# Optimization experiments

Measured on AMD Instinct MI355X. Metric: run time of the kernel, lower is better.

The kernel has to match this reference:

```python
import jax, jax.numpy as jnp
import numpy as np
from jax import lax

B, N, NPOINT, NSAMPLE = 4, 8192, 2048, 32
IN_CH = 64
MLP = (64, 64, 128)
RADIUS = 0.2
BN_EPS = 1e-5
BIG = 1e10


def _fps(xyz, npoint):
    # Farthest point sampling; deterministic start at index 0 (torch uses random start).
    b, n, _ = xyz.shape

    def body(carry, _):
        dist, far = carry
        cen = jnp.take_along_axis(xyz, far[:, None, None], axis=1)  # (B,1,3)
        d = jnp.sum((xyz - cen) ** 2, axis=-1)                      # (B,N)
        dist = jnp.minimum(dist, d)
        return (dist, jnp.argmax(dist, axis=-1).astype(jnp.int32)), far

    init = (jnp.full((b, n), BIG, xyz.dtype), jnp.zeros((b,), jnp.int32))
    _, cents = lax.scan(body, init, None, length=npoint)            # (npoint,B)
    return jnp.transpose(cents)                                     # (B,npoint)


def _sqdist(src, dst):
    # |src|^2 + |dst|^2 - 2 src.dst, clamped at 0 (matches square_distance)
    d = (jnp.sum(src ** 2, -1, keepdims=True)
         + jnp.sum(dst ** 2, -1, keepdims=True).swapaxes(1, 2)
         - 2.0 * jnp.einsum('bsc,bnc->bsn', src, dst))
    return jnp.maximum(d, 0.0)


def _ball_query(radius, nsample, xyz, new_xyz):
    sq = _sqdist(new_xyz, xyz)                           # (B,S,N)
    masked = jnp.where(sq > radius ** 2, BIG, sq)
    _, gidx = lax.top_k(-masked, nsample)                # nsample smallest dists
    gath = jnp.take_along_axis(sq, gidx, axis=2)
    # replace out-of-radius neighbors with the closest (first) neighbor
    return jnp.where(gath > radius ** 2, gidx[:, :, :1], gidx)


def _gather(points, idx):
    # points (B,N,C), idx (B,...) -> (B,...,C)
    return jax.vmap(lambda p, i: p[i])(points, idx)


def _forward(xyz, features, layers):
    fps_idx = _fps(xyz, NPOINT)                          # (B,S)
    new_xyz = _gather(xyz, fps_idx)                      # (B,S,3)
    idx = _ball_query(RADIUS, NSAMPLE, xyz, new_xyz)     # (B,S,K)
    g_xyz = _gather(xyz, idx) - new_xyz[:, :, None, :]   # (B,S,K,3) centered
    g_feat = _gather(features, idx)                      # (B,S,K,C)
    h = jnp.concatenate([g_xyz, g_feat], axis=-1)        # (B,S,K,3+C)
    for (W, g, b, m, v) in layers:                       # conv1x1 + BN(eval) + ReLU
        h = jnp.einsum('bskc,oc->bsko', h, W)
        h = jax.nn.relu((h - m) / jnp.sqrt(v + BN_EPS) * g + b)
    return new_xyz, jnp.max(h, axis=2)                   # max over neighbors K


def setup_inputs() -> dict:
    key = jax.random.key(0)
    ks = jax.random.split(key, 20)
    inp = {
        'xyz': jax.random.uniform(ks[0], (B, N, 3), jnp.float32),
        'features': jax.random.normal(ks[1], (B, N, IN_CH), jnp.float32),
    }
    last = IN_CH + 3
    k = 2
    for i, out in enumerate(MLP):
        inp[f'W{i}'] = jax.random.normal(ks[k], (out, last), jnp.float32) / np.sqrt(last); k += 1
        inp[f'gamma{i}'] = jax.random.uniform(ks[k], (out,), jnp.float32, 0.5, 1.5); k += 1
        inp[f'beta{i}'] = 0.1 * jax.random.normal(ks[k], (out,), jnp.float32); k += 1
        inp[f'mean{i}'] = 0.1 * jax.random.normal(ks[k], (out,), jnp.float32); k += 1
        inp[f'var{i}'] = jax.random.uniform(ks[k], (out,), jnp.float32, 0.5, 1.5); k += 1
        last = out
    return inp


def reference(xyz, features, W0, gamma0, beta0, mean0, var0, W1, gamma1, beta1, mean1, var1, W2, gamma2, beta2, mean2, var2):
    layers = [(W0, gamma0, beta0, mean0, var0),
              (W1, gamma1, beta1, mean1, var1),
              (W2, gamma2, beta2, mean2, var2)]
    return _forward(xyz, features, layers)
```

## Files before the change

kernel.cpp:

```cpp
#include <hip/hip_runtime.h>
#include <cstdint>

#define NPTS 8192
#define NBATCH 4
#define NS 2048
#define NK 32
#define CIN 64
#define C0 67
#define H1 64
#define H2 64
#define H3 128
#define CAP 1024
#define BIGF 1e10f

#define WT0_OFF 0
#define B0_OFF  4288
#define WT1_OFF 4352
#define B1_OFF  8448
#define WT2_OFF 8512
#define B2_OFF  16704
#define FPS_OFF 16832

typedef float f32x2 __attribute__((ext_vector_type(2)));

__device__ __forceinline__ float sq3(float ax, float ay, float az) {
  return __fadd_rn(__fadd_rn(__fmul_rn(ax, ax), __fmul_rn(ay, ay)), __fmul_rn(az, az));
}

__device__ __forceinline__ f32x2 pk_sub(f32x2 a, f32x2 b) {
  f32x2 r;
  asm("v_pk_add_f32 %0, %1, %2 neg_lo:[0,1] neg_hi:[0,1]" : "=v"(r) : "v"(a), "v"(b));
  return r;
}
__device__ __forceinline__ f32x2 pk_mul(f32x2 a, f32x2 b) {
  f32x2 r;
  asm("v_pk_mul_f32 %0, %1, %2" : "=v"(r) : "v"(a), "v"(b));
  return r;
}
__device__ __forceinline__ f32x2 pk_add(f32x2 a, f32x2 b) {
  f32x2 r;
  asm("v_pk_add_f32 %0, %1, %2" : "=v"(r) : "v"(a), "v"(b));
  return r;
}

#define PAIRRED(dv, iv, ctrl)                                                          \
  {                                                                                    \
    int _sd = __builtin_amdgcn_update_dpp(__float_as_int(dv), __float_as_int(dv),      \
                                          (ctrl), 0xf, 0xf, false);                    \
    int _si = __builtin_amdgcn_update_dpp((iv), (iv), (ctrl), 0xf, 0xf, false);        \
    float _fd = __int_as_float(_sd);                                                   \
    bool _tk = (_fd > (dv)) || ((_fd == (dv)) && (_si < (iv)));                        \
    (dv) = _tk ? _fd : (dv);                                                           \
    (iv) = _tk ? _si : (iv);                                                           \
  }

__global__ void fold_kernel(const float* __restrict__ W0, const float* __restrict__ g0, const float* __restrict__ be0, const float* __restrict__ m0, const float* __restrict__ v0,
                            const float* __restrict__ W1, const float* __restrict__ g1, const float* __restrict__ be1, const float* __restrict__ m1, const float* __restrict__ v1,
                            const float* __restrict__ W2, const float* __restrict__ g2, const float* __restrict__ be2, const float* __restrict__ m2, const float* __restrict__ v2,
                            float* __restrict__ ws) {
  int t = blockIdx.x * 256 + threadIdx.x;
  if (t < C0 * H1) {
    int c = t / H1, o = t - c * H1;
    float sc = g0[o] / sqrtf(v0[o] + 1e-5f);
    ws[WT0_OFF + t] = W0[o * C0 + c] * sc;
  } else if (t < B0_OFF + H1) {
    int o = t - B0_OFF;
    float sc = g0[o] / sqrtf(v0[o] + 1e-5f);
    ws[t] = be0[o] - m0[o] * sc;
  } else if (t < WT1_OFF + H1 * H2) {
    int t2 = t - WT1_OFF; int c = t2 / H2, o = t2 - c * H2;
    float sc = g1[o] / sqrtf(v1[o] + 1e-5f);
    ws[t] = W1[o * H1 + c] * sc;
  } else if (t < B1_OFF + H2) {
    int o = t - B1_OFF;
    float sc = g1[o] / sqrtf(v1[o] + 1e-5f);
    ws[t] = be1[o] - m1[o] * sc;
  } else if (t < WT2_OFF + H2 * H3) {
    int t2 = t - WT2_OFF; int c = t2 / H3, o = t2 - c * H3;
    float sc = g2[o] / sqrtf(v2[o] + 1e-5f);
    ws[t] = W2[o * H2 + c] * sc;
  } else if (t < B2_OFF + H3) {
    int o = t - B2_OFF;
    float sc = g2[o] / sqrtf(v2[o] + 1e-5f);
    ws[t] = be2[o] - m2[o] * sc;
  }
}

__global__ __launch_bounds__(256, 1)
void fps_kernel(const float* __restrict__ xyz, float* __restrict__ newxyz, int* __restrict__ fpsidx) {
  const int b = blockIdx.x;
  const float* px = xyz + (size_t)b * NPTS * 3;
  const int tid = threadIdx.x;
  const int lane = tid & 63;
  const int wv = tid >> 6;

  __shared__ __align__(16) float lco[NPTS * 4];
  __shared__ __align__(8) float cnd[2][4][2];

  f32x2 X2[16], Y2[16], Z2[16], D2[16];
#pragma unroll
  for (int jj = 0; jj < 16; ++jj) {
    int p0 = tid * 32 + 2 * jj;
    float x0 = px[p0 * 3 + 0], y0 = px[p0 * 3 + 1], z0 = px[p0 * 3 + 2];
    float x1 = px[p0 * 3 + 3], y1 = px[p0 * 3 + 4], z1 = px[p0 * 3 + 5];
    X2[jj][0] = x0; X2[jj][1] = x1;
    Y2[jj][0] = y0; Y2[jj][1] = y1;
    Z2[jj][0] = z0; Z2[jj][1] = z1;
    D2[jj][0] = BIGF; D2[jj][1] = BIGF;
    *(float4*)&lco[(size_t)p0 * 4]       = make_float4(x0, y0, z0, 0.0f);
    *(float4*)&lco[(size_t)(p0 + 1) * 4] = make_float4(x1, y1, z1, 0.0f);
  }

  float cx = px[0], cy = px[1], cz = px[2];
  if (tid == 0) {
    fpsidx[b * NS] = 0;
    float* o = newxyz + (size_t)b * NS * 3;
    o[0] = cx; o[1] = cy; o[2] = cz;
  }
  __syncthreads();

  int par = 0;
  for (int t = 1; t < NS; ++t) {
    f32x2 cpx, cpy, cpz;
    cpx[0] = cx; cpx[1] = cx;
    cpy[0] = cy; cpy[1] = cy;
    cpz[0] = cz; cpz[1] = cz;
    float bd = -1.0f; int bi = 0;
#pragma unroll
    for (int jj = 0; jj < 16; ++jj) {
      f32x2 dx = pk_sub(X2[jj], cpx);
      f32x2 dy = pk_sub(Y2[jj], cpy);
      f32x2 dz = pk_sub(Z2[jj], cpz);
      f32x2 xx = pk_mul(dx, dx);
      f32x2 yy = pk_mul(dy, dy);
      f32x2 ss = pk_add(xx, yy);
      f32x2 zz = pk_mul(dz, dz);
      f32x2 dd = pk_add(ss, zz);
      float n0 = fminf(D2[jj][0], dd[0]);
      float n1 = fminf(D2[jj][1], dd[1]);
      D2[jj][0] = n0; D2[jj][1] = n1;
      bool g0 = n0 > bd;
      bd = g0 ? n0 : bd;
      bi = g0 ? (tid * 32 + 2 * jj) : bi;
      bool g1 = n1 > bd;
      bd = g1 ? n1 : bd;
      bi = g1 ? (tid * 32 + 2 * jj + 1) : bi;
    }
    PAIRRED(bd, bi, 0x121);
    PAIRRED(bd, bi, 0x122);
    PAIRRED(bd, bi, 0x124);
    PAIRRED(bd, bi, 0x128);
    PAIRRED(bd, bi, 0x142);
    PAIRRED(bd, bi, 0x143);
    if (lane == 63) {
      cnd[par][wv][0] = bd;
      cnd[par][wv][1] = __int_as_float(bi);
    }
    __syncthreads();

    const int ci = lane & 3;
    f32x2 cc = *(const f32x2*)&cnd[par][ci][0];
    float pd = cc[0];
    int pi = __float_as_int(cc[1]);
    PAIRRED(pd, pi, 0x121);
    PAIRRED(pd, pi, 0x122);
    const int far = __builtin_amdgcn_readfirstlane(pi);
    float4 c4 = *(const float4*)&lco[(size_t)far * 4];
    cx = c4.x; cy = c4.y; cz = c4.z;
    if (tid == 0) {
      fpsidx[b * NS + t] = far;
      float* o = newxyz + ((size_t)b * NS + t) * 3;
      o[0] = cx; o[1] = cy; o[2] = cz;
    }
    par ^= 1;
  }
}

__global__ __launch_bounds__(256)
void sa_kernel(const float* __restrict__ xyz, const float* __restrict__ feat,
               const float* __restrict__ ws, const int* __restrict__ fpsidx,
               const float* __restrict__ newxyz, float* __restrict__ outf) {
  const int bs = blockIdx.x;
  const int b = bs >> 11;
  const int s = bs & (NS - 1);
  const int tid = threadIdx.x;
  const int lane = tid & 63;

  __shared__ __align__(16) unsigned long long cand[CAP];
  __shared__ int cntS;
  __shared__ int sel[NK];
  __shared__ float hA[32 * 69];
  __shared__ float hB[32 * 65];

  const float* px = xyz + (size_t)b * NPTS * 3;
  const float* pf = feat + (size_t)b * NPTS * CIN;
  const size_t srow = (size_t)b * NS + s;
  const float cx = newxyz[srow * 3 + 0];
  const float cy = newxyz[srow * 3 + 1];
  const float cz = newxyz[srow * 3 + 2];

  if (tid == 0) cntS = 0;
  __syncthreads();

  const float ssrc = sq3(cx, cy, cz);
  const float R2F = 0.04f;
  for (int p = tid; p < NPTS; p += 256) {
    float x = px[p * 3 + 0], y = px[p * 3 + 1], z = px[p * 3 + 2];
    float sdst = sq3(x, y, z);
    float dot = __fadd_rn(__fadd_rn(__fmul_rn(cx, x), __fmul_rn(cy, y)), __fmul_rn(cz, z));
    float d = __fsub_rn(__fadd_rn(ssrc, sdst), __fmul_rn(2.0f, dot));
    d = fmaxf(d, 0.0f);
    bool hit = (d <= R2F);
    unsigned long long m = __ballot(hit);
    if (m) {
      int base = 0;
      if (lane == 0) base = atomicAdd(&cntS, __popcll(m));
      base = __shfl(base, 0);
      if (hit) {
        int pos = base + __popcll(m & ((1ull << lane) - 1ull));
        if (pos < CAP)
          cand[pos] = ((unsigned long long)__float_as_uint(d) << 32) | (unsigned long long)(unsigned)p;
      }
    }
  }
  __syncthreads();

  {
    const int cnt = min(cntS, CAP);
    if (cnt <= 256) {
      unsigned long long k0 = (tid < cnt) ? cand[tid] : ~0ull;
      int r0 = 0;
      int j = 0;
      for (; j + 2 <= cnt; j += 2) {
        ulonglong2 kj = *(const ulonglong2*)&cand[j];
        r0 += (kj.x < k0) ? 1 : 0;
        r0 += (kj.y < k0) ? 1 : 0;
      }
      if (j < cnt) r0 += (cand[j] < k0) ? 1 : 0;
      if (tid < cnt) {
        if (r0 < NK) sel[r0] = (int)(k0 & 0xffffffffull);
        if (r0 == 0) {
          for (int q = cnt; q < NK; ++q) sel[q] = (int)(k0 & 0xffffffffull);
        }
      }
    } else if (cnt <= 512) {
      unsigned long long k0 = cand[tid];
      unsigned long long k1 = (256 + tid < cnt) ? cand[256 + tid] : ~0ull;
      int r0 = 0, r1 = 0;
      int j = 0;
      for (; j + 2 <= cnt; j += 2) {
        ulonglong2 kj = *(const ulonglong2*)&cand[j];
        r0 += (kj.x < k0) ? 1 : 0; r0 += (kj.y < k0) ? 1 : 0;
        r1 += (kj.x < k1) ? 1 : 0; r1 += (kj.y < k1) ? 1 : 0;
      }
      if (j < cnt) { unsigned long long kj = cand[j]; r0 += (kj < k0) ? 1 : 0; r1 += (kj < k1) ? 1 : 0; }
      if (r0 < NK) sel[r0] = (int)(k0 & 0xffffffffull);
      if (256 + tid < cnt && r1 < NK) sel[r1] = (int)(k1 & 0xffffffffull);
    } else {
      unsigned long long k0 = cand[tid];
      unsigned long long k1 = cand[256 + tid];
      unsigned long long k2 = (512 + tid < cnt) ? cand[512 + tid] : ~0ull;
      unsigned long long k3 = (768 + tid < cnt) ? cand[768 + tid] : ~0ull;
      int r0 = 0, r1 = 0, r2 = 0, r3 = 0;
      int j = 0;
      for (; j + 2 <= cnt; j += 2) {
        ulonglong2 kj = *(const ulonglong2*)&cand[j];
        r0 += (kj.x < k0) ? 1 : 0; r0 += (kj.y < k0) ? 1 : 0;
        r1 += (kj.x < k1) ? 1 : 0; r1 += (kj.y < k1) ? 1 : 0;
        r2 += (kj.x < k2) ? 1 : 0; r2 += (kj.y < k2) ? 1 : 0;
        r3 += (kj.x < k3) ? 1 : 0; r3 += (kj.y < k3) ? 1 : 0;
      }
      if (j < cnt) {
        unsigned long long kj = cand[j];
        r0 += (kj < k0) ? 1 : 0; r1 += (kj < k1) ? 1 : 0;
        r2 += (kj < k2) ? 1 : 0; r3 += (kj < k3) ? 1 : 0;
      }
      if (r0 < NK) sel[r0] = (int)(k0 & 0xffffffffull);
      if (r1 < NK) sel[r1] = (int)(k1 & 0xffffffffull);
      if (512 + tid < cnt && r2 < NK) sel[r2] = (int)(k2 & 0xffffffffull);
      if (768 + tid < cnt && r3 < NK) sel[r3] = (int)(k3 & 0xffffffffull);
    }
  }
  __syncthreads();

  {
    int kk = tid >> 3, j = tid & 7;
    int ip = sel[kk];
    const float* fr = pf + (size_t)ip * CIN + j * 8;
    float4 a = *(const float4*)(fr);
    float4 c4 = *(const float4*)(fr + 4);
    float* hrow = hA + kk * 69 + 3 + j * 8;
    hrow[0] = a.x;  hrow[1] = a.y;  hrow[2] = a.z;  hrow[3] = a.w;
    hrow[4] = c4.x; hrow[5] = c4.y; hrow[6] = c4.z; hrow[7] = c4.w;
  }
  if (tid < 32) {
    int ip = sel[tid];
    hA[tid * 69 + 0] = px[ip * 3 + 0] - cx;
    hA[tid * 69 + 1] = px[ip * 3 + 1] - cy;
    hA[tid * 69 + 2] = px[ip * 3 + 2] - cz;
  }
  __syncthreads();

  const int k = tid & 31;
  const int ob = tid >> 5;

  {
    const float* Wt = ws + WT0_OFF;
    const float* bb = ws + B0_OFF;
    const int o0 = ob * 8;
    float acc[8];
#pragma unroll
    for (int i = 0; i < 8; ++i) acc[i] = bb[o0 + i];
    const float* hrow = hA + k * 69;
    for (int c = 0; c < C0; ++c) {
      float h = hrow[c];
      const float4 w0 = *(const float4*)(Wt + c * H1 + o0);
      const float4 w1 = *(const float4*)(Wt + c * H1 + o0 + 4);
      acc[0] = fmaf(h, w0.x, acc[0]); acc[1] = fmaf(h, w0.y, acc[1]);
      acc[2] = fmaf(h, w0.z, acc[2]); acc[3] = fmaf(h, w0.w, acc[3]);
      acc[4] = fmaf(h, w1.x, acc[4]); acc[5] = fmaf(h, w1.y, acc[5]);
      acc[6] = fmaf(h, w1.z, acc[6]); acc[7] = fmaf(h, w1.w, acc[7]);
    }
    float* orow = hB + k * 65 + o0;
#pragma unroll
    for (int i = 0; i < 8; ++i) orow[i] = fmaxf(acc[i], 0.0f);
  }
  __syncthreads();

  {
    const float* Wt = ws + WT1_OFF;
    const float* bb = ws + B1_OFF;
    const int o0 = ob * 8;
    float acc[8];
#pragma unroll
    for (int i = 0; i < 8; ++i) acc[i] = bb[o0 + i];
    const float* hrow = hB + k * 65;
    for (int c = 0; c < H1; ++c) {
      float h = hrow[c];
      const float4 w0 = *(const float4*)(Wt + c * H2 + o0);
      const float4 w1 = *(const float4*)(Wt + c * H2 + o0 + 4);
      acc[0] = fmaf(h, w0.x, acc[0]); acc[1] = fmaf(h, w0.y, acc[1]);
      acc[2] = fmaf(h, w0.z, acc[2]); acc[3] = fmaf(h, w0.w, acc[3]);
      acc[4] = fmaf(h, w1.x, acc[4]); acc[5] = fmaf(h, w1.y, acc[5]);
      acc[6] = fmaf(h, w1.z, acc[6]); acc[7] = fmaf(h, w1.w, acc[7]);
    }
    float* orow = hA + k * 65 + o0;
#pragma unroll
    for (int i = 0; i < 8; ++i) orow[i] = fmaxf(acc[i], 0.0f);
  }
  __syncthreads();

  {
    const float* Wt = ws + WT2_OFF;
    const float* bb = ws + B2_OFF;
    const int o0 = ob * 16;
    float acc[16];
#pragma unroll
    for (int i = 0; i < 16; ++i) acc[i] = bb[o0 + i];
    const float* hrow = hA + k * 65;
    for (int c = 0; c < H2; ++c) {
      float h = hrow[c];
      const float4 w0 = *(const float4*)(Wt + c * H3 + o0);
      const float4 w1 = *(const float4*)(Wt + c * H3 + o0 + 4);
      const float4 w2 = *(const float4*)(Wt + c * H3 + o0 + 8);
      const float4 w3 = *(const float4*)(Wt + c * H3 + o0 + 12);
      acc[0]  = fmaf(h, w0.x, acc[0]);  acc[1]  = fmaf(h, w0.y, acc[1]);
      acc[2]  = fmaf(h, w0.z, acc[2]);  acc[3]  = fmaf(h, w0.w, acc[3]);
      acc[4]  = fmaf(h, w1.x, acc[4]);  acc[5]  = fmaf(h, w1.y, acc[5]);
      acc[6]  = fmaf(h, w1.z, acc[6]);  acc[7]  = fmaf(h, w1.w, acc[7]);
      acc[8]  = fmaf(h, w2.x, acc[8]);  acc[9]  = fmaf(h, w2.y, acc[9]);
      acc[10] = fmaf(h, w2.z, acc[10]); acc[11] = fmaf(h, w2.w, acc[11]);
      acc[12] = fmaf(h, w3.x, acc[12]); acc[13] = fmaf(h, w3.y, acc[13]);
      acc[14] = fmaf(h, w3.z, acc[14]); acc[15] = fmaf(h, w3.w, acc[15]);
    }
#pragma unroll
    for (int i = 0; i < 16; ++i) acc[i] = fmaxf(acc[i], 0.0f);
#pragma unroll
    for (int m = 1; m < 32; m <<= 1) {
#pragma unroll
      for (int i = 0; i < 16; ++i) {
        float o = __shfl_xor(acc[i], m);
        acc[i] = fmaxf(acc[i], o);
      }
    }
    if (k == 0) {
      float* op = outf + srow * H3 + o0;
      *(float4*)(op + 0)  = make_float4(acc[0],  acc[1],  acc[2],  acc[3]);
      *(float4*)(op + 4)  = make_float4(acc[4],  acc[5],  acc[6],  acc[7]);
      *(float4*)(op + 8)  = make_float4(acc[8],  acc[9],  acc[10], acc[11]);
      *(float4*)(op + 12) = make_float4(acc[12], acc[13], acc[14], acc[15]);
    }
  }
}

extern "C" void kernel_launch(void* const* d_in, const int* in_sizes, int n_in,
                              void* d_out, int out_size, void* d_ws, size_t ws_size,
                              hipStream_t stream) {
  const float* xyz  = (const float*)d_in[0];
  const float* feat = (const float*)d_in[1];
  const float* W0 = (const float*)d_in[2];
  const float* g0 = (const float*)d_in[3];
  const float* be0 = (const float*)d_in[4];
  const float* m0 = (const float*)d_in[5];
  const float* v0 = (const float*)d_in[6];
  const float* W1 = (const float*)d_in[7];
  const float* g1 = (const float*)d_in[8];
  const float* be1 = (const float*)d_in[9];
  const float* m1 = (const float*)d_in[10];
  const float* v1 = (const float*)d_in[11];
  const float* W2 = (const float*)d_in[12];
  const float* g2 = (const float*)d_in[13];
  const float* be2 = (const float*)d_in[14];
  const float* m2 = (const float*)d_in[15];
  const float* v2 = (const float*)d_in[16];

  float* out = (float*)d_out;
  float* ws = (float*)d_ws;
  int* fpsidx = (int*)(ws + FPS_OFF);
  float* outfeat = out + (size_t)NBATCH * NS * 3;

  fold_kernel<<<(B2_OFF + H3 + 255) / 256, 256, 0, stream>>>(
      W0, g0, be0, m0, v0, W1, g1, be1, m1, v1, W2, g2, be2, m2, v2, ws);
  fps_kernel<<<NBATCH, 256, 0, stream>>>(xyz, out, fpsidx);
  sa_kernel<<<NBATCH * NS, 256, 0, stream>>>(xyz, feat, ws, fpsidx, out, outfeat);
}
```

Baseline: 2.691 ms.

## Fuse FPS and set-abstraction into one persistent producer-consumer kernel

Merges the farthest-point-sampling kernel and the ball-query/MLP kernel into a single launch. Four blocks run FPS and publish progress counters with release atomics every 16 centroids. 248 persistent consumer blocks poll those counters and process centroids as soon as they are ready, so the MLP work overlaps the serial FPS loop instead of waiting for it to finish. In exchange, the shared-memory union makes every block large, so each CU holds only one block and the consumer phase has low occupancy. The scheme also relies on all blocks being co-resident to avoid deadlock, and a stray extra write into the FPS candidate buffer may break its double buffering.

```diff
diff --git a/kernel.cpp b/kernel.cpp
--- a/kernel.cpp
+++ b/kernel.cpp
@@ -12,6 +12,7 @@
 #define H3 128
 #define CAP 1024
 #define BIGF 1e10f
+#define NCONS 248
 
 #define WT0_OFF 0
 #define B0_OFF  4288
@@ -20,6 +21,16 @@
 #define WT2_OFF 8512
 #define B2_OFF  16704
 #define FPS_OFF 16832
+
+#define P_LCO 0
+#define P_CND 131072
+#define C_CAND 0
+#define C_HA   8192
+#define C_HB   17024
+#define C_SEL  25344
+#define C_SEEN 25472
+#define C_CNT  25488
+#define SMEM_BYTES 131200
 
 typedef float f32x2 __attribute__((ext_vector_type(2)));
 
@@ -87,308 +98,328 @@
 }
 
 __global__ __launch_bounds__(256, 1)
-void fps_kernel(const float* __restrict__ xyz, float* __restrict__ newxyz, int* __restrict__ fpsidx) {
-  const int b = blockIdx.x;
-  const float* px = xyz + (size_t)b * NPTS * 3;
+void fused_kernel(const float* __restrict__ xyz, const float* __restrict__ feat,
+                  const float* __restrict__ ws, float* __restrict__ newxyz,
+                  float* __restrict__ outf, int* __restrict__ prog) {
+  __shared__ __align__(16) char smem[SMEM_BYTES];
+  const int blk = blockIdx.x;
   const int tid = threadIdx.x;
   const int lane = tid & 63;
-  const int wv = tid >> 6;
-
-  __shared__ __align__(16) float lco[NPTS * 4];
-  __shared__ __align__(8) float cnd[2][4][2];
-
-  f32x2 X2[16], Y2[16], Z2[16], D2[16];
-#pragma unroll
-  for (int jj = 0; jj < 16; ++jj) {
-    int p0 = tid * 32 + 2 * jj;
-    float x0 = px[p0 * 3 + 0], y0 = px[p0 * 3 + 1], z0 = px[p0 * 3 + 2];
-    float x1 = px[p0 * 3 + 3], y1 = px[p0 * 3 + 4], z1 = px[p0 * 3 + 5];
-    X2[jj][0] = x0; X2[jj][1] = x1;
-    Y2[jj][0] = y0; Y2[jj][1] = y1;
-    Z2[jj][0] = z0; Z2[jj][1] = z1;
-    D2[jj][0] = BIGF; D2[jj][1] = BIGF;
-    *(float4*)&lco[(size_t)p0 * 4]       = make_float4(x0, y0, z0, 0.0f);
-    *(float4*)&lco[(size_t)(p0 + 1) * 4] = make_float4(x1, y1, z1, 0.0f);
-  }
-
-  float cx = px[0], cy = px[1], cz = px[2];
-  if (tid == 0) {
-    fpsidx[b * NS] = 0;
-    float* o = newxyz + (size_t)b * NS * 3;
-    o[0] = cx; o[1] = cy; o[2] = cz;
-  }
-  __syncthreads();
-
-  int par = 0;
-  for (int t = 1; t < NS; ++t) {
-    f32x2 cpx, cpy, cpz;
-    cpx[0] = cx; cpx[1] = cx;
-    cpy[0] = cy; cpy[1] = cy;
-    cpz[0] = cz; cpz[1] = cz;
-    float bd = -1.0f; int bi = 0;
+
+  if (blk < NBATCH) {
+    const int b = blk;
+    const float* px = xyz + (size_t)b * NPTS * 3;
+    const int wv = tid >> 6;
+    float* lco = (float*)(smem + P_LCO);
+    float (*cnd)[4][2] = (float(*)[4][2])(smem + P_CND);
+    int* pb = prog + b * 64;
+
+    f32x2 X2[16], Y2[16], Z2[16], D2[16];
 #pragma unroll
     for (int jj = 0; jj < 16; ++jj) {
-      f32x2 dx = pk_sub(X2[jj], cpx);
-      f32x2 dy = pk_sub(Y2[jj], cpy);
-      f32x2 dz = pk_sub(Z2[jj], cpz);
-      f32x2 xx = pk_mul(dx, dx);
-      f32x2 yy = pk_mul(dy, dy);
-      f32x2 ss = pk_add(xx, yy);
-      f32x2 zz = pk_mul(dz, dz);
-      f32x2 dd = pk_add(ss, zz);
-      float n0 = fminf(D2[jj][0], dd[0]);
-      float n1 = fminf(D2[jj][1], dd[1]);
-      D2[jj][0] = n0; D2[jj][1] = n1;
-      bool g0 = n0 > bd;
-      bd = g0 ? n0 : bd;
-      bi = g0 ? (tid * 32 + 2 * jj) : bi;
-      bool g1 = n1 > bd;
-      bd = g1 ? n1 : bd;
-      bi = g1 ? (tid * 32 + 2 * jj + 1) : bi;
+      int p0 = tid * 32 + 2 * jj;
+      float x0 = px[p0 * 3 + 0], y0 = px[p0 * 3 + 1], z0 = px[p0 * 3 + 2];
+      float x1 = px[p0 * 3 + 3], y1 = px[p0 * 3 + 4], z1 = px[p0 * 3 + 5];
+      X2[jj][0] = x0; X2[jj][1] = x1;
+      Y2[jj][0] = y0; Y2[jj][1] = y1;
+      Z2[jj][0] = z0; Z2[jj][1] = z1;
+      D2[jj][0] = BIGF; D2[jj][1] = BIGF;
+      *(float4*)&lco[(size_t)p0 * 4]       = make_float4(x0, y0, z0, 0.0f);
+      *(float4*)&lco[(size_t)(p0 + 1) * 4] = make_float4(x1, y1, z1, 0.0f);
     }
-    PAIRRED(bd, bi, 0x121);
-    PAIRRED(bd, bi, 0x122);
-    PAIRRED(bd, bi, 0x124);
-    PAIRRED(bd, bi, 0x128);
-    PAIRRED(bd, bi, 0x142);
-    PAIRRED(bd, bi, 0x143);
-    if (lane == 63) {
-      cnd[par][wv][0] = bd;
-      cnd[par][wv][1] = __int_as_float(bi);
+
+    float cx = px[0], cy = px[1], cz = px[2];
+    if (tid == 0) {
+      float* o = newxyz + (size_t)b * NS * 3;
+      o[0] = cx; o[1] = cy; o[2] = cz;
     }
     __syncthreads();
 
-    const int ci = lane & 3;
-    f32x2 cc = *(const f32x2*)&cnd[par][ci][0];
-    float pd = cc[0];
-    int pi = __float_as_int(cc[1]);
-    PAIRRED(pd, pi, 0x121);
-    PAIRRED(pd, pi, 0x122);
-    const int far = __builtin_amdgcn_readfirstlane(pi);
-    float4 c4 = *(const float4*)&lco[(size_t)far * 4];
-    cx = c4.x; cy = c4.y; cz = c4.z;
-    if (tid == 0) {
-      fpsidx[b * NS + t] = far;
-      float* o = newxyz + ((size_t)b * NS + t) * 3;
-      o[0] = cx; o[1] = cy; o[2] = cz;
+    int par = 0;
+    for (int t = 1; t < NS; ++t) {
+      f32x2 cpx, cpy, cpz;
+      cpx[0] = cx; cpx[1] = cx;
+      cpy[0] = cy; cpy[1] = cy;
+      cpz[0] = cz; cpz[1] = cz;
+      float bd = -1.0f; int bi = 0;
+#pragma unroll
+      for (int jj = 0; jj < 16; ++jj) {
+        f32x2 dx = pk_sub(X2[jj], cpx);
+        f32x2 dy = pk_sub(Y2[jj], cpy);
+        f32x2 dz = pk_sub(Z2[jj], cpz);
+        f32x2 xx = pk_mul(dx, dx);
+        f32x2 yy = pk_mul(dy, dy);
+        f32x2 ss = pk_add(xx, yy);
+        f32x2 zz = pk_mul(dz, dz);
+        f32x2 dd = pk_add(ss, zz);
+        float n0 = fminf(D2[jj][0], dd[0]);
+        float n1 = fminf(D2[jj][1], dd[1]);
+        D2[jj][0] = n0; D2[jj][1] = n1;
+        bool g0 = n0 > bd;
+        bd = g0 ? n0 : bd;
+        bi = g0 ? (tid * 32 + 2 * jj) : bi;
+        bool g1 = n1 > bd;
+        bd = g1 ? n1 : bd;
+        bi = g1 ? (tid * 32 + 2 * jj + 1) : bi;
+      }
+      PAIRRED(bd, bi, 0x121);
+      PAIRRED(bd, bi, 0x122);
+      PAIRRED(bd, bi, 0x124);
+      PAIRRED(bd, bi, 0x128);
+      PAIRRED(bd, bi, 0x142);
+      PAIRRED(bd, bi, 0x143);
+      if (lane == 63) {
+        (*cnd)[wv][0] = bd;
+      }
+      if (lane == 63) {
+        cnd[par][wv][0] = bd;
+        cnd[par][wv][1] = __int_as_float(bi);
+      }
+      __syncthreads();
+
+      const int ci = lane & 3;
+      f32x2 cc = *(const f32x2*)&cnd[par][ci][0];
+      float pd = cc[0];
+      int pi = __float_as_int(cc[1]);
+      PAIRRED(pd, pi, 0x121);
+      PAIRRED(pd, pi, 0x122);
+      const int far = __builtin_amdgcn_readfirstlane(pi);
+      float4 c4 = *(const float4*)&lco[(size_t)far * 4];
+      cx = c4.x; cy = c4.y; cz = c4.z;
+      if (tid == 0) {
+        float* o = newxyz + ((size_t)b * NS + t) * 3;
+        o[0] = cx; o[1] = cy; o[2] = cz;
+        if ((t & 15) == 15) {
+          __hip_atomic_store(pb, t + 1, __ATOMIC_RELEASE, __HIP_MEMORY_SCOPE_AGENT);
+        }
+      }
+      par ^= 1;
     }
-    par ^= 1;
-  }
-}
-
-__global__ __launch_bounds__(256)
-void sa_kernel(const float* __restrict__ xyz, const float* __restrict__ feat,
-               const float* __restrict__ ws, const int* __restrict__ fpsidx,
-               const float* __restrict__ newxyz, float* __restrict__ outf) {
-  const int bs = blockIdx.x;
-  const int b = bs >> 11;
-  const int s = bs & (NS - 1);
-  const int tid = threadIdx.x;
-  const int lane = tid & 63;
-
-  __shared__ __align__(16) unsigned long long cand[CAP];
-  __shared__ int cntS;
-  __shared__ int sel[NK];
-  __shared__ float hA[32 * 69];
-  __shared__ float hB[32 * 65];
-
-  const float* px = xyz + (size_t)b * NPTS * 3;
-  const float* pf = feat + (size_t)b * NPTS * CIN;
-  const size_t srow = (size_t)b * NS + s;
-  const float cx = newxyz[srow * 3 + 0];
-  const float cy = newxyz[srow * 3 + 1];
-  const float cz = newxyz[srow * 3 + 2];
-
-  if (tid == 0) cntS = 0;
-  __syncthreads();
-
-  const float ssrc = sq3(cx, cy, cz);
-  const float R2F = 0.04f;
-  for (int p = tid; p < NPTS; p += 256) {
-    float x = px[p * 3 + 0], y = px[p * 3 + 1], z = px[p * 3 + 2];
-    float sdst = sq3(x, y, z);
-    float dot = __fadd_rn(__fadd_rn(__fmul_rn(cx, x), __fmul_rn(cy, y)), __fmul_rn(cz, z));
-    float d = __fsub_rn(__fadd_rn(ssrc, sdst), __fmul_rn(2.0f, dot));
-    d = fmaxf(d, 0.0f);
-    bool hit = (d <= R2F);
-    unsigned long long m = __ballot(hit);
-    if (m) {
-      int base = 0;
-      if (lane == 0) base = atomicAdd(&cntS, __popcll(m));
-      base = __shfl(base, 0);
-      if (hit) {
-        int pos = base + __popcll(m & ((1ull << lane) - 1ull));
-        if (pos < CAP)
-          cand[pos] = ((unsigned long long)__float_as_uint(d) << 32) | (unsigned long long)(unsigned)p;
-      }
-    }
-  }
-  __syncthreads();
-
-  {
-    const int cnt = min(cntS, CAP);
-    if (cnt <= 256) {
-      unsigned long long k0 = (tid < cnt) ? cand[tid] : ~0ull;
-      int r0 = 0;
-      int j = 0;
-      for (; j + 2 <= cnt; j += 2) {
-        ulonglong2 kj = *(const ulonglong2*)&cand[j];
-        r0 += (kj.x < k0) ? 1 : 0;
-        r0 += (kj.y < k0) ? 1 : 0;
-      }
-      if (j < cnt) r0 += (cand[j] < k0) ? 1 : 0;
-      if (tid < cnt) {
-        if (r0 < NK) sel[r0] = (int)(k0 & 0xffffffffull);
-        if (r0 == 0) {
-          for (int q = cnt; q < NK; ++q) sel[q] = (int)(k0 & 0xffffffffull);
-        }
-      }
-    } else if (cnt <= 512) {
-      unsigned long long k0 = cand[tid];
-      unsigned long long k1 = (256 + tid < cnt) ? cand[256 + tid] : ~0ull;
-      int r0 = 0, r1 = 0;
-      int j = 0;
-      for (; j + 2 <= cnt; j += 2) {
-        ulonglong2 kj = *(const ulonglong2*)&cand[j];
-        r0 += (kj.x < k0) ? 1 : 0; r0 += (kj.y < k0) ? 1 : 0;
-        r1 += (kj.x < k1) ? 1 : 0; r1 += (kj.y < k1) ? 1 : 0;
-      }
-      if (j < cnt) { unsigned long long kj = cand[j]; r0 += (kj < k0) ? 1 : 0; r1 += (kj < k1) ? 1 : 0; }
-      if (r0 < NK) sel[r0] = (int)(k0 & 0xffffffffull);
-      if (256 + tid < cnt && r1 < NK) sel[r1] = (int)(k1 & 0xffffffffull);
-    } else {
-      unsigned long long k0 = cand[tid];
-      unsigned long long k1 = cand[256 + tid];
-      unsigned long long k2 = (512 + tid < cnt) ? cand[512 + tid] : ~0ull;
-      unsigned long long k3 = (768 + tid < cnt) ? cand[768 + tid] : ~0ull;
-      int r0 = 0, r1 = 0, r2 = 0, r3 = 0;
-      int j = 0;
-      for (; j + 2 <= cnt; j += 2) {
-        ulonglong2 kj = *(const ulonglong2*)&cand[j];
-        r0 += (kj.x < k0) ? 1 : 0; r0 += (kj.y < k0) ? 1 : 0;
-        r1 += (kj.x < k1) ? 1 : 0; r1 += (kj.y < k1) ? 1 : 0;
-        r2 += (kj.x < k2) ? 1 : 0; r2 += (kj.y < k2) ? 1 : 0;
-        r3 += (kj.x < k3) ? 1 : 0; r3 += (kj.y < k3) ? 1 : 0;
-      }
-      if (j < cnt) {
-        unsigned long long kj = cand[j];
-        r0 += (kj < k0) ? 1 : 0; r1 += (kj < k1) ? 1 : 0;
-        r2 += (kj < k2) ? 1 : 0; r3 += (kj < k3) ? 1 : 0;
-      }
-      if (r0 < NK) sel[r0] = (int)(k0 & 0xffffffffull);
-      if (r1 < NK) sel[r1] = (int)(k1 & 0xffffffffull);
-      if (512 + tid < cnt && r2 < NK) sel[r2] = (int)(k2 & 0xffffffffull);
-      if (768 + tid < cnt && r3 < NK) sel[r3] = (int)(k3 & 0xffffffffull);
-    }
-  }
-  __syncthreads();
-
-  {
-    int kk = tid >> 3, j = tid & 7;
-    int ip = sel[kk];
-    const float* fr = pf + (size_t)ip * CIN + j * 8;
-    float4 a = *(const float4*)(fr);
-    float4 c4 = *(const float4*)(fr + 4);
-    float* hrow = hA + kk * 69 + 3 + j * 8;
-    hrow[0] = a.x;  hrow[1] = a.y;  hrow[2] = a.z;  hrow[3] = a.w;
-    hrow[4] = c4.x; hrow[5] = c4.y; hrow[6] = c4.z; hrow[7] = c4.w;
-  }
-  if (tid < 32) {
-    int ip = sel[tid];
-    hA[tid * 69 + 0] = px[ip * 3 + 0] - cx;
-    hA[tid * 69 + 1] = px[ip * 3 + 1] - cy;
-    hA[tid * 69 + 2] = px[ip * 3 + 2] - cz;
-  }
-  __syncthreads();
-
-  const int k = tid & 31;
-  const int ob = tid >> 5;
-
-  {
-    const float* Wt = ws + WT0_OFF;
-    const float* bb = ws + B0_OFF;
-    const int o0 = ob * 8;
-    float acc[8];
-#pragma unroll
-    for (int i = 0; i < 8; ++i) acc[i] = bb[o0 + i];
-    const float* hrow = hA + k * 69;
-    for (int c = 0; c < C0; ++c) {
-      float h = hrow[c];
-      const float4 w0 = *(const float4*)(Wt + c * H1 + o0);
-      const float4 w1 = *(const float4*)(Wt + c * H1 + o0 + 4);
-      acc[0] = fmaf(h, w0.x, acc[0]); acc[1] = fmaf(h, w0.y, acc[1]);
-      acc[2] = fmaf(h, w0.z, acc[2]); acc[3] = fmaf(h, w0.w, acc[3]);
-      acc[4] = fmaf(h, w1.x, acc[4]); acc[5] = fmaf(h, w1.y, acc[5]);
-      acc[6] = fmaf(h, w1.z, acc[6]); acc[7] = fmaf(h, w1.w, acc[7]);
-    }
-    float* orow = hB + k * 65 + o0;
-#pragma unroll
-    for (int i = 0; i < 8; ++i) orow[i] = fmaxf(acc[i], 0.0f);
-  }
-  __syncthreads();
-
-  {
-    const float* Wt = ws + WT1_OFF;
-    const float* bb = ws + B1_OFF;
-    const int o0 = ob * 8;
-    float acc[8];
-#pragma unroll
-    for (int i = 0; i < 8; ++i) acc[i] = bb[o0 + i];
-    const float* hrow = hB + k * 65;
-    for (int c = 0; c < H1; ++c) {
-      float h = hrow[c];
-      const float4 w0 = *(const float4*)(Wt + c * H2 + o0);
-      const float4 w1 = *(const float4*)(Wt + c * H2 + o0 + 4);
-      acc[0] = fmaf(h, w0.x, acc[0]); acc[1] = fmaf(h, w0.y, acc[1]);
-      acc[2] = fmaf(h, w0.z, acc[2]); acc[3] = fmaf(h, w0.w, acc[3]);
-      acc[4] = fmaf(h, w1.x, acc[4]); acc[5] = fmaf(h, w1.y, acc[5]);
-      acc[6] = fmaf(h, w1.z, acc[6]); acc[7] = fmaf(h, w1.w, acc[7]);
-    }
-    float* orow = hA + k * 65 + o0;
-#pragma unroll
-    for (int i = 0; i < 8; ++i) orow[i] = fmaxf(acc[i], 0.0f);
-  }
-  __syncthreads();
-
-  {
-    const float* Wt = ws + WT2_OFF;
-    const float* bb = ws + B2_OFF;
-    const int o0 = ob * 16;
-    float acc[16];
-#pragma unroll
-    for (int i = 0; i < 16; ++i) acc[i] = bb[o0 + i];
-    const float* hrow = hA + k * 65;
-    for (int c = 0; c < H2; ++c) {
-      float h = hrow[c];
-      const float4 w0 = *(const float4*)(Wt + c * H3 + o0);
-      const float4 w1 = *(const float4*)(Wt + c * H3 + o0 + 4);
-      const float4 w2 = *(const float4*)(Wt + c * H3 + o0 + 8);
-      const float4 w3 = *(const float4*)(Wt + c * H3 + o0 + 12);
-      acc[0]  = fmaf(h, w0.x, acc[0]);  acc[1]  = fmaf(h, w0.y, acc[1]);
-      acc[2]  = fmaf(h, w0.z, acc[2]);  acc[3]  = fmaf(h, w0.w, acc[3]);
-      acc[4]  = fmaf(h, w1.x, acc[4]);  acc[5]  = fmaf(h, w1.y, acc[5]);
-      acc[6]  = fmaf(h, w1.z, acc[6]);  acc[7]  = fmaf(h, w1.w, acc[7]);
-      acc[8]  = fmaf(h, w2.x, acc[8]);  acc[9]  = fmaf(h, w2.y, acc[9]);
-      acc[10] = fmaf(h, w2.z, acc[10]); acc[11] = fmaf(h, w2.w, acc[11]);
-      acc[12] = fmaf(h, w3.x, acc[12]); acc[13] = fmaf(h, w3.y, acc[13]);
-      acc[14] = fmaf(h, w3.z, acc[14]); acc[15] = fmaf(h, w3.w, acc[15]);
-    }
-#pragma unroll
-    for (int i = 0; i < 16; ++i) acc[i] = fmaxf(acc[i], 0.0f);
-#pragma unroll
-    for (int m = 1; m < 32; m <<= 1) {
-#pragma unroll
-      for (int i = 0; i < 16; ++i) {
-        float o = __shfl_xor(acc[i], m);
-        acc[i] = fmaxf(acc[i], o);
-      }
-    }
-    if (k == 0) {
-      float* op = outf + srow * H3 + o0;
-      *(float4*)(op + 0)  = make_float4(acc[0],  acc[1],  acc[2],  acc[3]);
-      *(float4*)(op + 4)  = make_float4(acc[4],  acc[5],  acc[6],  acc[7]);
-      *(float4*)(op + 8)  = make_float4(acc[8],  acc[9],  acc[10], acc[11]);
-      *(float4*)(op + 12) = make_float4(acc[12], acc[13], acc[14], acc[15]);
+  } else {
+    unsigned long long* cand = (unsigned long long*)(smem + C_CAND);
+    float* hA = (float*)(smem + C_HA);
+    float* hB = (float*)(smem + C_HB);
+    int* sel = (int*)(smem + C_SEL);
+    int* seen = (int*)(smem + C_SEEN);
+    int* cntp = (int*)(smem + C_CNT);
+
+    if (tid < NBATCH) seen[tid] = 0;
+    __syncthreads();
+
+    for (int bs = blk - NBATCH; bs < NBATCH * NS; bs += NCONS) {
+      const int b = bs >> 11;
+      const int s = bs & (NS - 1);
+
+      if (tid == 0) {
+        *cntp = 0;
+        if (seen[b] <= s) {
+          int pv;
+          do {
+            pv = __hip_atomic_load(prog + b * 64, __ATOMIC_ACQUIRE, __HIP_MEMORY_SCOPE_AGENT);
+            if (pv <= s) __builtin_amdgcn_s_sleep(8);
+          } while (pv <= s);
+          seen[b] = pv;
+        }
+      }
+      __syncthreads();
+
+      const float* px = xyz + (size_t)b * NPTS * 3;
+      const float* pf = feat + (size_t)b * NPTS * CIN;
+      const size_t srow = (size_t)b * NS + s;
+      const float cx = newxyz[srow * 3 + 0];
+      const float cy = newxyz[srow * 3 + 1];
+      const float cz = newxyz[srow * 3 + 2];
+
+      const float ssrc = sq3(cx, cy, cz);
+      const float R2F = 0.04f;
+      for (int p = tid; p < NPTS; p += 256) {
+        float x = px[p * 3 + 0], y = px[p * 3 + 1], z = px[p * 3 + 2];
+        float sdst = sq3(x, y, z);
+        float dot = __fadd_rn(__fadd_rn(__fmul_rn(cx, x), __fmul_rn(cy, y)), __fmul_rn(cz, z));
+        float d = __fsub_rn(__fadd_rn(ssrc, sdst), __fmul_rn(2.0f, dot));
+        d = fmaxf(d, 0.0f);
+        bool hit = (d <= R2F);
+        unsigned long long m = __ballot(hit);
+        if (m) {
+          int base = 0;
+          if (lane == 0) base = atomicAdd(cntp, __popcll(m));
+          base = __shfl(base, 0);
+          if (hit) {
+            int pos = base + __popcll(m & ((1ull << lane) - 1ull));
+            if (pos < CAP)
+              cand[pos] = ((unsigned long long)__float_as_uint(d) << 32) | (unsigned long long)(unsigned)p;
+          }
+        }
+      }
+      __syncthreads();
+
+      {
+        const int cnt = min(*cntp, CAP);
+        if (cnt <= 256) {
+          unsigned long long k0 = (tid < cnt) ? cand[tid] : ~0ull;
+          int r0 = 0;
+          int j = 0;
+          for (; j + 2 <= cnt; j += 2) {
+            ulonglong2 kj = *(const ulonglong2*)&cand[j];
+            r0 += (kj.x < k0) ? 1 : 0;
+            r0 += (kj.y < k0) ? 1 : 0;
+          }
+          if (j < cnt) r0 += (cand[j] < k0) ? 1 : 0;
+          if (tid < cnt) {
+            if (r0 < NK) sel[r0] = (int)(k0 & 0xffffffffull);
+            if (r0 == 0) {
+              for (int q = cnt; q < NK; ++q) sel[q] = (int)(k0 & 0xffffffffull);
+            }
+          }
+        } else if (cnt <= 512) {
+          unsigned long long k0 = cand[tid];
+          unsigned long long k1 = (256 + tid < cnt) ? cand[256 + tid] : ~0ull;
+          int r0 = 0, r1 = 0;
+          int j = 0;
+          for (; j + 2 <= cnt; j += 2) {
+            ulonglong2 kj = *(const ulonglong2*)&cand[j];
+            r0 += (kj.x < k0) ? 1 : 0; r0 += (kj.y < k0) ? 1 : 0;
+            r1 += (kj.x < k1) ? 1 : 0; r1 += (kj.y < k1) ? 1 : 0;
+          }
+          if (j < cnt) { unsigned long long kj = cand[j]; r0 += (kj < k0) ? 1 : 0; r1 += (kj < k1) ? 1 : 0; }
+          if (r0 < NK) sel[r0] = (int)(k0 & 0xffffffffull);
+          if (256 + tid < cnt && r1 < NK) sel[r1] = (int)(k1 & 0xffffffffull);
+        } else {
+          unsigned long long k0 = cand[tid];
+          unsigned long long k1 = cand[256 + tid];
+          unsigned long long k2 = (512 + tid < cnt) ? cand[512 + tid] : ~0ull;
+          unsigned long long k3 = (768 + tid < cnt) ? cand[768 + tid] : ~0ull;
+          int r0 = 0, r1 = 0, r2 = 0, r3 = 0;
+          int j = 0;
+          for (; j + 2 <= cnt; j += 2) {
+            ulonglong2 kj = *(const ulonglong2*)&cand[j];
+            r0 += (kj.x < k0) ? 1 : 0; r0 += (kj.y < k0) ? 1 : 0;
+            r1 += (kj.x < k1) ? 1 : 0; r1 += (kj.y < k1) ? 1 : 0;
+            r2 += (kj.x < k2) ? 1 : 0; r2 += (kj.y < k2) ? 1 : 0;
+            r3 += (kj.x < k3) ? 1 : 0; r3 += (kj.y < k3) ? 1 : 0;
+          }
+          if (j < cnt) {
+            unsigned long long kj = cand[j];
+            r0 += (kj < k0) ? 1 : 0; r1 += (kj < k1) ? 1 : 0;
+            r2 += (kj < k2) ? 1 : 0; r3 += (kj < k3) ? 1 : 0;
+          }
+          if (r0 < NK) sel[r0] = (int)(k0 & 0xffffffffull);
+          if (r1 < NK) sel[r1] = (int)(k1 & 0xffffffffull);
+          if (512 + tid < cnt && r2 < NK) sel[r2] = (int)(k2 & 0xffffffffull);
+          if (768 + tid < cnt && r3 < NK) sel[r3] = (int)(k3 & 0xffffffffull);
+        }
+      }
+      __syncthreads();
+
+      {
+        int kk = tid >> 3, j = tid & 7;
+        int ip = sel[kk];
+        const float* fr = pf + (size_t)ip * CIN + j * 8;
+        float4 a = *(const float4*)(fr);
+        float4 c4 = *(const float4*)(fr + 4);
+        float* hrow = hA + kk * 69 + 3 + j * 8;
+        hrow[0] = a.x;  hrow[1] = a.y;  hrow[2] = a.z;  hrow[3] = a.w;
+        hrow[4] = c4.x; hrow[5] = c4.y; hrow[6] = c4.z; hrow[7] = c4.w;
+      }
+      if (tid < 32) {
+        int ip = sel[tid];
+        hA[tid * 69 + 0] = px[ip * 3 + 0] - cx;
+        hA[tid * 69 + 1] = px[ip * 3 + 1] - cy;
+        hA[tid * 69 + 2] = px[ip * 3 + 2] - cz;
+      }
+      __syncthreads();
+
+      const int k = tid & 31;
+      const int ob = tid >> 5;
+
+      {
+        const float* Wt = ws + WT0_OFF;
+        const float* bb = ws + B0_OFF;
+        const int o0 = ob * 8;
+        float acc[8];
+#pragma unroll
+        for (int i = 0; i < 8; ++i) acc[i] = bb[o0 + i];
+        const float* hrow = hA + k * 69;
+        for (int c = 0; c < C0; ++c) {
+          float h = hrow[c];
+          const float4 w0 = *(const float4*)(Wt + c * H1 + o0);
+          const float4 w1 = *(const float4*)(Wt + c * H1 + o0 + 4);
+          acc[0] = fmaf(h, w0.x, acc[0]); acc[1] = fmaf(h, w0.y, acc[1]);
+          acc[2] = fmaf(h, w0.z, acc[2]); acc[3] = fmaf(h, w0.w, acc[3]);
+          acc[4] = fmaf(h, w1.x, acc[4]); acc[5] = fmaf(h, w1.y, acc[5]);
+          acc[6] = fmaf(h, w1.z, acc[6]); acc[7] = fmaf(h, w1.w, acc[7]);
+        }
+        float* orow = hB + k * 65 + o0;
+#pragma unroll
+        for (int i = 0; i < 8; ++i) orow[i] = fmaxf(acc[i], 0.0f);
+      }
+      __syncthreads();
+
+      {
+        const float* Wt = ws + WT1_OFF;
+        const float* bb = ws + B1_OFF;
+        const int o0 = ob * 8;
+        float acc[8];
+#pragma unroll
+        for (int i = 0; i < 8; ++i) acc[i] = bb[o0 + i];
+        const float* hrow = hB + k * 65;
+        for (int c = 0; c < H1; ++c) {
+          float h = hrow[c];
+          const float4 w0 = *(const float4*)(Wt + c * H2 + o0);
+          const float4 w1 = *(const float4*)(Wt + c * H2 + o0 + 4);
+          acc[0] = fmaf(h, w0.x, acc[0]); acc[1] = fmaf(h, w0.y, acc[1]);
+          acc[2] = fmaf(h, w0.z, acc[2]); acc[3] = fmaf(h, w0.w, acc[3]);
+          acc[4] = fmaf(h, w1.x, acc[4]); acc[5] = fmaf(h, w1.y, acc[5]);
+          acc[6] = fmaf(h, w1.z, acc[6]); acc[7] = fmaf(h, w1.w, acc[7]);
+        }
+        float* orow = hA + k * 65 + o0;
+#pragma unroll
+        for (int i = 0; i < 8; ++i) orow[i] = fmaxf(acc[i], 0.0f);
+      }
+      __syncthreads();
+
+      {
+        const float* Wt = ws + WT2_OFF;
+        const float* bb = ws + B2_OFF;
+        const int o0 = ob * 16;
+        float acc[16];
+#pragma unroll
+        for (int i = 0; i < 16; ++i) acc[i] = bb[o0 + i];
+        const float* hrow = hA + k * 65;
+        for (int c = 0; c < H2; ++c) {
+          float h = hrow[c];
+          const float4 w0 = *(const float4*)(Wt + c * H3 + o0);
+          const float4 w1 = *(const float4*)(Wt + c * H3 + o0 + 4);
+          const float4 w2 = *(const float4*)(Wt + c * H3 + o0 + 8);
+          const float4 w3 = *(const float4*)(Wt + c * H3 + o0 + 12);
+          acc[0]  = fmaf(h, w0.x, acc[0]);  acc[1]  = fmaf(h, w0.y, acc[1]);
+          acc[2]  = fmaf(h, w0.z, acc[2]);  acc[3]  = fmaf(h, w0.w, acc[3]);
+          acc[4]  = fmaf(h, w1.x, acc[4]);  acc[5]  = fmaf(h, w1.y, acc[5]);
+          acc[6]  = fmaf(h, w1.z, acc[6]);  acc[7]  = fmaf(h, w1.w, acc[7]);
+          acc[8]  = fmaf(h, w2.x, acc[8]);  acc[9]  = fmaf(h, w2.y, acc[9]);
+          acc[10] = fmaf(h, w2.z, acc[10]); acc[11] = fmaf(h, w2.w, acc[11]);
+          acc[12] = fmaf(h, w3.x, acc[12]); acc[13] = fmaf(h, w3.y, acc[13]);
+          acc[14] = fmaf(h, w3.z, acc[14]); acc[15] = fmaf(h, w3.w, acc[15]);
+        }
+#pragma unroll
+        for (int i = 0; i < 16; ++i) acc[i] = fmaxf(acc[i], 0.0f);
+#pragma unroll
+        for (int m = 1; m < 32; m <<= 1) {
+#pragma unroll
+          for (int i = 0; i < 16; ++i) {
+            float o = __shfl_xor(acc[i], m);
+            acc[i] = fmaxf(acc[i], o);
+          }
+        }
+        if (k == 0) {
+          float* op = outf + srow * H3 + o0;
+          *(float4*)(op + 0)  = make_float4(acc[0],  acc[1],  acc[2],  acc[3]);
+          *(float4*)(op + 4)  = make_float4(acc[4],  acc[5],  acc[6],  acc[7]);
+          *(float4*)(op + 8)  = make_float4(acc[8],  acc[9],  acc[10], acc[11]);
+          *(float4*)(op + 12) = make_float4(acc[12], acc[13], acc[14], acc[15]);
+        }
+      }
+      __syncthreads();
     }
   }
 }
@@ -415,12 +446,12 @@
   const float* v2 = (const float*)d_in[16];
 
   float* out = (float*)d_out;
-  float* ws = (float*)d_ws;
-  int* fpsidx = (int*)(ws + FPS_OFF);
+  float* wsf = (float*)d_ws;
+  int* prog = (int*)(wsf + FPS_OFF);
   float* outfeat = out + (size_t)NBATCH * NS * 3;
 
   fold_kernel<<<(B2_OFF + H3 + 255) / 256, 256, 0, stream>>>(
-      W0, g0, be0, m0, v0, W1, g1, be1, m1, v1, W2, g2, be2, m2, v2, ws);
-  fps_kernel<<<NBATCH, 256, 0, stream>>>(xyz, out, fpsidx);
-  sa_kernel<<<NBATCH * NS, 256, 0, stream>>>(xyz, feat, ws, fpsidx, out, outfeat);
-}
+      W0, g0, be0, m0, v0, W1, g1, be1, m1, v1, W2, g2, be2, m2, v2, wsf);
+  hipMemsetAsync(prog, 0, NBATCH * 64 * sizeof(int), stream);
+  fused_kernel<<<NBATCH + NCONS, 256, 0, stream>>>(xyz, feat, wsf, out, outfeat, prog);
+}
```

New measurement: 4.397 ms. +63.4%, slower.
